# Performance work log

Measured on AMD Instinct MI355X. Metric: run time of the kernel, lower is better.

The kernel has to match this reference:

```python
import jax, jax.numpy as jnp
import numpy as np

D_MODEL = 1024
SCALE = float(np.sqrt(D_MODEL))


def setup_inputs() -> dict:
    key = jax.random.key(0)
    k1, k2, k3 = jax.random.split(key, 3)
    input_data = jax.random.normal(k1, (4, 2048, D_MODEL), dtype=jnp.float32)
    qk = jax.random.normal(k2, (D_MODEL, D_MODEL), dtype=jnp.float32) / SCALE
    ov = jax.random.normal(k3, (D_MODEL, D_MODEL), dtype=jnp.float32) / SCALE
    return {"input_data": input_data, "qk": qk, "ov": ov}


def reference(input_data, qk, ov):
    # input_data: [B, S, D]; qk, ov: [D, D]
    S = input_data.shape[1]
    # scores: [B, S, S] = (x @ qk) @ x^T / sqrt(D)
    scores = jnp.einsum("bsd,de,bte->bst", input_data, qk, input_data) / SCALE
    # causal mask: positions t > s get -inf (upper triangle, diagonal=1)
    causal = jnp.tril(jnp.ones((S, S), dtype=bool))
    scores = jnp.where(causal, scores, -jnp.inf)
    attn = jax.nn.softmax(scores, axis=-1)
    # A: [B, S, D] = attn @ x @ ov
    return jnp.einsum("bst,btd,de->bse", attn, input_data, ov)
```

## Files before the change

kernel.cpp:

```cpp
#include <hip/hip_runtime.h>
#include <hip/hip_bf16.h>
#include <cstdint>
#include <cstddef>
#include <type_traits>


using bf16 = __hip_bfloat16;
typedef __attribute__((ext_vector_type(8))) short short8;
typedef __attribute__((ext_vector_type(4))) float f32x4;

#define NB 4
#define SS 2048
#define DD 1024

__device__ __forceinline__ void async_lds16(const bf16* g, bf16* l) {
  __builtin_amdgcn_global_load_lds(
      (const __attribute__((address_space(1))) void*)g,
      (__attribute__((address_space(3))) void*)l,
      16, 0, 0);
}

struct alignas(8) bf16x4s { bf16 a, b, c, d; };

__global__ __launch_bounds__(256) void prep_kernel(const float* __restrict__ x,
                                                   bf16* __restrict__ xb,
                                                   const float* __restrict__ qk,
                                                   bf16* __restrict__ qkT,
                                                   const float* __restrict__ ov,
                                                   bf16* __restrict__ ovT,
                                                   float* __restrict__ l) {
  __shared__ bf16 tile[64][65];
  const int bx = blockIdx.x;
  if (bx < 8192) {
    int i = (bx * 256 + threadIdx.x) * 4;
    float4 v = *(const float4*)(x + i);
    bf16x4s o{__float2bfloat16(v.x), __float2bfloat16(v.y),
              __float2bfloat16(v.z), __float2bfloat16(v.w)};
    *(bf16x4s*)(xb + i) = o;
  } else if (bx < 8704) {
    const int idx = bx - 8192;
    const float* in = (idx & 256) ? ov : qk;
    bf16* out = (idx & 256) ? ovT : qkT;
    const int rem = idx & 255;
    const int tbx = (rem & 15) * 64;
    const int tby = (rem >> 4) * 64;
    const int tc = threadIdx.x & 63;
    const int tr = threadIdx.x >> 6;
#pragma unroll
    for (int r = tr; r < 64; r += 4)
      tile[tc][r] = __float2bfloat16(in[(size_t)(tby + r) * DD + tbx + tc]);
    __syncthreads();
#pragma unroll
    for (int r = tr; r < 64; r += 4)
      out[(size_t)(tbx + r) * DD + tby + tc] = tile[r][tc];
  } else {
    const int t = (bx - 8704) * 256 + threadIdx.x;
    f32x4 z = {0.f, 0.f, 0.f, 0.f};
    *(f32x4*)(l + t * 4) = z;
  }
}

template <int EPI>
__device__ __forceinline__ void gemm256_core(const bf16* __restrict__ Ab,
                                             const bf16* __restrict__ Bb,
                                             void* __restrict__ C,
                                             int N, int K, int m0, int n0, int nk,
                                             bf16* As, bf16* Bs,
                                             float* __restrict__ l) {
  const int lane = threadIdx.x & 63;
  const int wave = threadIdx.x >> 6;
  const int wr   = wave >> 2;
  const int wc   = wave & 3;
  const int quad = lane >> 4;
  const int r    = lane & 15;

  f32x4 acc[8][4];
#pragma unroll
  for (int i = 0; i < 8; ++i)
#pragma unroll
    for (int n = 0; n < 4; ++n) acc[i][n] = f32x4{0.f, 0.f, 0.f, 0.f};

  const int lrow = lane >> 3;
  const int lsw  = (lane & 7) ^ lrow;
  const long long a_lane = (long long)(m0 + wave * 8 + lrow) * K + lsw * 8;
  const long long b_lane = (long long)(n0 + wave * 8 + lrow) * K + lsw * 8;

  auto stageA = [&](int kt, int rnd, int buf) {
    async_lds16(Ab + a_lane + (long long)(rnd * 64) * K + (long long)kt * 64,
                As + buf * 16384 + (rnd * 64 + wave * 8) * 64);
  };
  auto stageB = [&](int kt, int rnd, int buf) {
    async_lds16(Bb + b_lane + (long long)(rnd * 64) * K + (long long)kt * 64,
                Bs + buf * 16384 + (rnd * 64 + wave * 8) * 64);
  };

  stageA(0, 0, 0); stageA(0, 2, 0);
  stageB(0, 0, 0); stageB(0, 1, 0); stageB(0, 2, 0); stageB(0, 3, 0);
  stageA(0, 1, 0); stageA(0, 3, 0);
  asm volatile("s_waitcnt vmcnt(2)" ::: "memory");
  asm volatile("s_barrier" ::: "memory");

  const int ca0 = (quad ^ (r & 7)) * 8;
  const int ca1 = ((4 + quad) ^ (r & 7)) * 8;

  for (int kt = 0; kt < nk; ++kt) {
    const int buf = kt & 1, nxt = buf ^ 1;
    const bool hn = (kt + 1 < nk);
    const bf16* Abuf = As + buf * 16384 + (wr * 128) * 64;
    const bf16* Bbuf = Bs + buf * 16384 + (wc * 64) * 64;

    auto phase = [&](auto RHC, int ca, auto&& stg, int wmode) {
      constexpr int RH = decltype(RHC)::value;
      short8 af[4], bfr[4];
#pragma unroll
      for (int m = 0; m < 4; ++m)
        af[m] = *(const short8*)(Abuf + (RH * 64 + m * 16 + r) * 64 + ca);
#pragma unroll
      for (int n = 0; n < 4; ++n)
        bfr[n] = *(const short8*)(Bbuf + (n * 16 + r) * 64 + ca);
      stg();
      asm volatile("s_barrier" ::: "memory");
      asm volatile("s_waitcnt lgkmcnt(0)" ::: "memory");
      __builtin_amdgcn_sched_barrier(0);
      __builtin_amdgcn_s_setprio(1);
#pragma unroll
      for (int m = 0; m < 4; ++m)
#pragma unroll
        for (int n = 0; n < 4; ++n)
          acc[RH * 4 + m][n] = __builtin_amdgcn_mfma_f32_16x16x32_bf16(
              af[m], bfr[n], acc[RH * 4 + m][n], 0, 0, 0);
      __builtin_amdgcn_s_setprio(0);
      if (wmode == 1) {
        if (hn) asm volatile("s_waitcnt vmcnt(2)" ::: "memory");
        else    asm volatile("s_waitcnt vmcnt(0)" ::: "memory");
      } else if (wmode == 2) {
        if (hn) asm volatile("s_waitcnt vmcnt(2)" ::: "memory");
      }
      asm volatile("s_barrier" ::: "memory");
    };

    phase(std::integral_constant<int, 0>{}, ca0,
          [&] { if (hn) { stageA(kt + 1, 0, nxt); stageA(kt + 1, 2, nxt); } }, 1);
    phase(std::integral_constant<int, 1>{}, ca0,
          [&] { if (hn) { stageB(kt + 1, 0, nxt); stageB(kt + 1, 1, nxt); } }, 0);
    phase(std::integral_constant<int, 0>{}, ca1,
          [&] { if (hn) { stageB(kt + 1, 2, nxt); stageB(kt + 1, 3, nxt); } }, 0);
    phase(std::integral_constant<int, 1>{}, ca1,
          [&] { if (hn) { stageA(kt + 1, 1, nxt); stageA(kt + 1, 3, nxt); } }, 2);
  }

#pragma unroll
  for (int i = 0; i < 8; ++i) {
    const int row0 = m0 + wr * 128 + i * 16 + quad * 4;
    if (EPI == 1) {
#pragma unroll
      for (int n = 0; n < 4; ++n) {
        const int col = n0 + wc * 64 + n * 16 + r;
#pragma unroll
        for (int q = 0; q < 4; ++q)
          ((bf16*)C)[(long long)(row0 + q) * N + col] = __float2bfloat16(acc[i][n][q]);
      }
    } else if (EPI == 2) {
      float qs[4] = {0.f, 0.f, 0.f, 0.f};
#pragma unroll
      for (int n = 0; n < 4; ++n) {
        const int col = n0 + wc * 64 + n * 16 + r;
#pragma unroll
        for (int q = 0; q < 4; ++q) {
          const int row = row0 + q;
          float v = (col <= row) ? __expf(acc[i][n][q] * 0.03125f) : 0.0f;
          ((bf16*)C)[(long long)row * N + col] = __float2bfloat16(v);
          qs[q] += v;
        }
      }
#pragma unroll
      for (int q = 0; q < 4; ++q) {
#pragma unroll
        for (int off = 1; off < 16; off <<= 1) qs[q] += __shfl_xor(qs[q], off, 64);
        if (r == 0) atomicAdd(&l[row0 + q], qs[q]);
      }
    } else {
      float rs[4];
#pragma unroll
      for (int q = 0; q < 4; ++q) rs[q] = 1.0f / l[row0 + q];
#pragma unroll
      for (int n = 0; n < 4; ++n) {
        const int col = n0 + wc * 64 + n * 16 + r;
#pragma unroll
        for (int q = 0; q < 4; ++q)
          ((float*)C)[(long long)(row0 + q) * N + col] = acc[i][n][q] * rs[q];
      }
    }
  }
}

__global__ __launch_bounds__(512, 2) void gemm_qv256(const bf16* __restrict__ xb,
                                                     const bf16* __restrict__ qkT,
                                                     const bf16* __restrict__ ovT,
                                                     bf16* __restrict__ Qb,
                                                     bf16* __restrict__ Vt) {
  extern __shared__ bf16 lds[];
  bf16* As = lds;
  bf16* Bs = lds + 32768;
  const long long SD = (long long)SS * DD;
  const int z = blockIdx.z;
  if (z < 4) {
    const int bn = blockIdx.x & 3, bm = blockIdx.x >> 2;
    gemm256_core<1>(xb + z * SD, qkT, Qb + z * SD, DD, DD, bm * 256, bn * 256, 16,
                    As, Bs, nullptr);
  } else {
    const int bm = blockIdx.x & 3, bn = blockIdx.x >> 2;
    gemm256_core<1>(ovT, xb + (z - 4) * SD, Vt + (z - 4) * SD, SS, DD, bm * 256, bn * 256, 16,
                    As, Bs, nullptr);
  }
}

__global__ __launch_bounds__(512, 2) void gemm_sc256(const bf16* __restrict__ Qb,
                                                     const bf16* __restrict__ xb,
                                                     bf16* __restrict__ P,
                                                     float* __restrict__ l) {
  extern __shared__ bf16 lds[];
  bf16* As = lds;
  bf16* Bs = lds + 32768;
  const long long SD = (long long)SS * DD;
  const long long SSQ = (long long)SS * SS;
  const int t = blockIdx.x;
  int bm = (int)((sqrtf(8.0f * (float)t + 1.0f) - 1.0f) * 0.5f);
  while ((bm + 1) * (bm + 2) / 2 <= t) ++bm;
  while (bm * (bm + 1) / 2 > t) --bm;
  const int bn = t - bm * (bm + 1) / 2;
  const int b = blockIdx.z;
  gemm256_core<2>(Qb + b * SD, xb + b * SD, P + b * SSQ, SS, DD, bm * 256, bn * 256, 16,
                  As, Bs, l + b * SS);
}

__global__ __launch_bounds__(512, 2) void gemm_pv256(const bf16* __restrict__ P,
                                                     const bf16* __restrict__ Vt,
                                                     const float* __restrict__ l,
                                                     float* __restrict__ out) {
  extern __shared__ bf16 lds[];
  bf16* As = lds;
  bf16* Bs = lds + 32768;
  const long long SD = (long long)SS * DD;
  const long long SSQ = (long long)SS * SS;
  const int bx = blockIdx.x & 3;
  const int bm = blockIdx.x >> 2;
  const int b = blockIdx.z;
  gemm256_core<3>(P + b * SSQ, Vt + b * SD, out + b * SD, DD, SS,
                  bm * 256, bx * 256, 4 * (bm + 1), As, Bs, (float*)l + b * SS);
}

extern "C" void kernel_launch(void* const* d_in, const int* in_sizes, int n_in,
                              void* d_out, int out_size, void* d_ws, size_t ws_size,
                              hipStream_t stream) {
  const float* x  = (const float*)d_in[0];
  const float* qk = (const float*)d_in[1];
  const float* ov = (const float*)d_in[2];
  float* out = (float*)d_out;

  char* ws = (char*)d_ws;
  const size_t MB = 1ull << 20;
  bf16*  xb  = (bf16*)(ws + 0);
  bf16*  qkT = (bf16*)(ws + 16 * MB);
  bf16*  ovT = (bf16*)(ws + 18 * MB);
  bf16*  Qb  = (bf16*)(ws + 20 * MB);
  bf16*  Vt  = (bf16*)(ws + 36 * MB);
  bf16*  P   = (bf16*)(ws + 52 * MB);
  float* l   = (float*)(ws + 84 * MB);

  static bool lds_opt_in = false;
  if (!lds_opt_in) {
    hipFuncSetAttribute((const void*)gemm_qv256,
                        hipFuncAttributeMaxDynamicSharedMemorySize, 131072);
    hipFuncSetAttribute((const void*)gemm_sc256,
                        hipFuncAttributeMaxDynamicSharedMemorySize, 131072);
    hipFuncSetAttribute((const void*)gemm_pv256,
                        hipFuncAttributeMaxDynamicSharedMemorySize, 131072);
    lds_opt_in = true;
  }

  prep_kernel<<<dim3(8712), 256, 0, stream>>>(x, xb, qk, qkT, ov, ovT, l);
  gemm_qv256<<<dim3(32, 1, 8), 512, 131072, stream>>>(xb, qkT, ovT, Qb, Vt);
  gemm_sc256<<<dim3(36, 1, 4), 512, 131072, stream>>>(Qb, xb, P, l);
  gemm_pv256<<<dim3(32, 1, 4), 512, 131072, stream>>>(P, Vt, l, out);
}
```

Before: 217.0 us.

## Triple-buffer A tiles in LDS to prefetch two k-steps ahead

Grows the A-operand LDS staging from two buffers to three, so A tiles are fetched two k-iterations ahead while B stays double-buffered. The per-phase staging schedule and vmcnt waits are reworked to match, and dynamic LDS grows to 160 KB per block. The aim is to hide more global-load latency behind MFMA work, at the cost of more LDS per block. That may cut occupancy: with launch_bounds(512,2) two blocks can no longer fit on a CU's LDS.

Result: slower. 221.8 us (+2.2%).

```diff
diff --git a/kernel.cpp b/kernel.cpp
--- a/kernel.cpp
+++ b/kernel.cpp
@@ -94,22 +94,30 @@
                 Bs + buf * 16384 + (rnd * 64 + wave * 8) * 64);
   };
 
-  stageA(0, 0, 0); stageA(0, 2, 0);
+  stageA(0, 0, 0); stageA(0, 2, 0); stageA(0, 1, 0); stageA(0, 3, 0);
   stageB(0, 0, 0); stageB(0, 1, 0); stageB(0, 2, 0); stageB(0, 3, 0);
-  stageA(0, 1, 0); stageA(0, 3, 0);
-  asm volatile("s_waitcnt vmcnt(2)" ::: "memory");
+  if (nk > 1) {
+    stageA(1, 0, 1); stageA(1, 2, 1); stageA(1, 1, 1); stageA(1, 3, 1);
+    asm volatile("s_waitcnt vmcnt(4)" ::: "memory");
+  } else {
+    asm volatile("s_waitcnt vmcnt(0)" ::: "memory");
+  }
   asm volatile("s_barrier" ::: "memory");
 
   const int ca0 = (quad ^ (r & 7)) * 8;
   const int ca1 = ((4 + quad) ^ (r & 7)) * 8;
 
+  int ba = 0;
   for (int kt = 0; kt < nk; ++kt) {
-    const int buf = kt & 1, nxt = buf ^ 1;
-    const bool hn = (kt + 1 < nk);
-    const bf16* Abuf = As + buf * 16384 + (wr * 128) * 64;
-    const bf16* Bbuf = Bs + buf * 16384 + (wc * 64) * 64;
-
-    auto phase = [&](auto RHC, int ca, auto&& stg, int wmode) {
+    const int bb  = kt & 1;
+    const int bb1 = bb ^ 1;
+    int ba2 = ba + 2; if (ba2 >= 3) ba2 -= 3;
+    const bool hnA = (kt + 2 < nk);
+    const bool hnB = (kt + 1 < nk);
+    const bf16* Abuf = As + ba * 16384 + (wr * 128) * 64;
+    const bf16* Bbuf = Bs + bb * 16384 + (wc * 64) * 64;
+
+    auto phase = [&](auto RHC, int ca, auto&& stg, bool tail) {
       constexpr int RH = decltype(RHC)::value;
       short8 af[4], bfr[4];
 #pragma unroll
@@ -130,23 +138,25 @@
           acc[RH * 4 + m][n] = __builtin_amdgcn_mfma_f32_16x16x32_bf16(
               af[m], bfr[n], acc[RH * 4 + m][n], 0, 0, 0);
       __builtin_amdgcn_s_setprio(0);
-      if (wmode == 1) {
-        if (hn) asm volatile("s_waitcnt vmcnt(2)" ::: "memory");
-        else    asm volatile("s_waitcnt vmcnt(0)" ::: "memory");
-      } else if (wmode == 2) {
-        if (hn) asm volatile("s_waitcnt vmcnt(2)" ::: "memory");
+      if (tail) {
+        if (hnA)      asm volatile("s_waitcnt vmcnt(2)" ::: "memory");
+        else if (hnB) asm volatile("s_waitcnt vmcnt(0)" ::: "memory");
       }
       asm volatile("s_barrier" ::: "memory");
     };
 
     phase(std::integral_constant<int, 0>{}, ca0,
-          [&] { if (hn) { stageA(kt + 1, 0, nxt); stageA(kt + 1, 2, nxt); } }, 1);
+          [&] {
+            if (hnA) { stageA(kt + 2, 0, ba2); stageA(kt + 2, 2, ba2); }
+            if (hnB) { stageB(kt + 1, 0, bb1); stageB(kt + 1, 1, bb1); }
+          }, false);
     phase(std::integral_constant<int, 1>{}, ca0,
-          [&] { if (hn) { stageB(kt + 1, 0, nxt); stageB(kt + 1, 1, nxt); } }, 0);
-    phase(std::integral_constant<int, 0>{}, ca1,
-          [&] { if (hn) { stageB(kt + 1, 2, nxt); stageB(kt + 1, 3, nxt); } }, 0);
+          [&] { if (hnB) { stageB(kt + 1, 2, bb1); stageB(kt + 1, 3, bb1); } }, false);
+    phase(std::integral_constant<int, 0>{}, ca1, [&] {}, false);
     phase(std::integral_constant<int, 1>{}, ca1,
-          [&] { if (hn) { stageA(kt + 1, 1, nxt); stageA(kt + 1, 3, nxt); } }, 2);
+          [&] { if (hnA) { stageA(kt + 2, 1, ba2); stageA(kt + 2, 3, ba2); } }, true);
+
+    if (++ba == 3) ba = 0;
   }
 
 #pragma unroll
@@ -201,7 +211,7 @@
                                                      bf16* __restrict__ Vt) {
   extern __shared__ bf16 lds[];
   bf16* As = lds;
-  bf16* Bs = lds + 32768;
+  bf16* Bs = lds + 49152;
   const long long SD = (long long)SS * DD;
   const int z = blockIdx.z;
   if (z < 4) {
@@ -221,7 +231,7 @@
                                                      float* __restrict__ l) {
   extern __shared__ bf16 lds[];
   bf16* As = lds;
-  bf16* Bs = lds + 32768;
+  bf16* Bs = lds + 49152;
   const long long SD = (long long)SS * DD;
   const long long SSQ = (long long)SS * SS;
   const int t = blockIdx.x;
@@ -240,7 +250,7 @@
                                                      float* __restrict__ out) {
   extern __shared__ bf16 lds[];
   bf16* As = lds;
-  bf16* Bs = lds + 32768;
+  bf16* Bs = lds + 49152;
   const long long SD = (long long)SS * DD;
   const long long SSQ = (long long)SS * SS;
   const int bx = blockIdx.x & 3;
@@ -271,16 +281,16 @@
   static bool lds_opt_in = false;
   if (!lds_opt_in) {
     hipFuncSetAttribute((const void*)gemm_qv256,
-                        hipFuncAttributeMaxDynamicSharedMemorySize, 131072);
+                        hipFuncAttributeMaxDynamicSharedMemorySize, 163840);
     hipFuncSetAttribute((const void*)gemm_sc256,
-                        hipFuncAttributeMaxDynamicSharedMemorySize, 131072);
+                        hipFuncAttributeMaxDynamicSharedMemorySize, 163840);
     hipFuncSetAttribute((const void*)gemm_pv256,
-                        hipFuncAttributeMaxDynamicSharedMemorySize, 131072);
+                        hipFuncAttributeMaxDynamicSharedMemorySize, 163840);
     lds_opt_in = true;
   }
 
   prep_kernel<<<dim3(8712), 256, 0, stream>>>(x, xb, qk, qkT, ov, ovT, l);
-  gemm_qv256<<<dim3(32, 1, 8), 512, 131072, stream>>>(xb, qkT, ovT, Qb, Vt);
-  gemm_sc256<<<dim3(36, 1, 4), 512, 131072, stream>>>(Qb, xb, P, l);
-  gemm_pv256<<<dim3(32, 1, 4), 512, 131072, stream>>>(P, Vt, l, out);
-}
+  gemm_qv256<<<dim3(32, 1, 8), 512, 163840, stream>>>(xb, qkT, ovT, Qb, Vt);
+  gemm_sc256<<<dim3(36, 1, 4), 512, 163840, stream>>>(Qb, xb, P, l);
+  gemm_pv256<<<dim3(32, 1, 4), 512, 163840, stream>>>(P, Vt, l, out);
+}
```

## Rewrite PV GEMM with 128-tile core and paired causal row blocks

Applied to the files above, without the earlier changes.

Replaces the 256x256 PV GEMM with a new 128x128 tile core using 256 threads, triple-buffered A and double-buffered B async LDS staging. Each block processes two complementary causal row tiles (row pr and 15-pr), so every block does the same total K work and the triangular imbalance disappears. The launch grows to 256 blocks, which gives more parallelism across CUs. In exchange, the smaller tiles reuse each loaded element less and the new pipeline code is more complex.

After: 192.7 us. 11.2% less time.

```diff
diff --git a/kernel.cpp b/kernel.cpp
--- a/kernel.cpp
+++ b/kernel.cpp
@@ -179,17 +179,108 @@
         for (int off = 1; off < 16; off <<= 1) qs[q] += __shfl_xor(qs[q], off, 64);
         if (r == 0) atomicAdd(&l[row0 + q], qs[q]);
       }
-    } else {
-      float rs[4];
-#pragma unroll
-      for (int q = 0; q < 4; ++q) rs[q] = 1.0f / l[row0 + q];
-#pragma unroll
-      for (int n = 0; n < 4; ++n) {
-        const int col = n0 + wc * 64 + n * 16 + r;
-#pragma unroll
-        for (int q = 0; q < 4; ++q)
-          ((float*)C)[(long long)(row0 + q) * N + col] = acc[i][n][q] * rs[q];
-      }
+    }
+  }
+}
+
+__device__ __forceinline__ void gemm128_core(const bf16* __restrict__ Ab,
+                                             const bf16* __restrict__ Bb,
+                                             float* __restrict__ C,
+                                             const float* __restrict__ l,
+                                             int N, int K, int m0, int n0, int nk,
+                                             bf16* As, bf16* Bs) {
+  const int lane = threadIdx.x & 63;
+  const int wave = threadIdx.x >> 6;
+  const int wr   = wave >> 1;
+  const int wc   = wave & 1;
+  const int quad = lane >> 4;
+  const int r    = lane & 15;
+
+  f32x4 acc[4][4];
+#pragma unroll
+  for (int m = 0; m < 4; ++m)
+#pragma unroll
+    for (int n = 0; n < 4; ++n) acc[m][n] = f32x4{0.f, 0.f, 0.f, 0.f};
+
+  const int lrow = lane >> 3;
+  const int lsw  = (lane & 7) ^ lrow;
+  const long long a_base = (long long)(m0 + wave * 32 + lrow) * K + lsw * 8;
+  const long long b_base = (long long)(n0 + wave * 32 + lrow) * K + lsw * 8;
+
+  auto stageA = [&](int kt, int buf) {
+#pragma unroll
+    for (int i = 0; i < 4; ++i)
+      async_lds16(Ab + a_base + (long long)(i * 8) * K + (long long)kt * 64,
+                  As + buf * 8192 + (wave * 32 + i * 8) * 64);
+  };
+  auto stageB = [&](int kt, int buf) {
+#pragma unroll
+    for (int i = 0; i < 4; ++i)
+      async_lds16(Bb + b_base + (long long)(i * 8) * K + (long long)kt * 64,
+                  Bs + buf * 8192 + (wave * 32 + i * 8) * 64);
+  };
+
+  stageB(0, 0); stageA(0, 0); stageA(1, 1);
+  asm volatile("s_waitcnt vmcnt(4)" ::: "memory");
+  asm volatile("s_barrier" ::: "memory");
+
+  const int ca0 = (quad ^ (r & 7)) * 8;
+  const int ca1 = ((4 + quad) ^ (r & 7)) * 8;
+
+  int ba = 0;
+  for (int kt = 0; kt < nk; ++kt) {
+    const int bb = kt & 1;
+    int ba2 = ba + 2; if (ba2 >= 3) ba2 -= 3;
+    const bool hA = (kt + 2 < nk), hB = (kt + 1 < nk);
+    const bf16* Abuf = As + ba * 8192;
+    const bf16* Bbuf = Bs + bb * 8192;
+
+    auto phase = [&](int ca, auto&& stg, bool tail) {
+      short8 af[4], bfr[4];
+#pragma unroll
+      for (int m = 0; m < 4; ++m)
+        af[m] = *(const short8*)(Abuf + (wr * 64 + m * 16 + r) * 64 + ca);
+#pragma unroll
+      for (int n = 0; n < 4; ++n)
+        bfr[n] = *(const short8*)(Bbuf + (wc * 64 + n * 16 + r) * 64 + ca);
+      stg();
+      asm volatile("s_barrier" ::: "memory");
+      asm volatile("s_waitcnt lgkmcnt(0)" ::: "memory");
+      __builtin_amdgcn_sched_barrier(0);
+      __builtin_amdgcn_s_setprio(1);
+#pragma unroll
+      for (int m = 0; m < 4; ++m)
+#pragma unroll
+        for (int n = 0; n < 4; ++n)
+          acc[m][n] = __builtin_amdgcn_mfma_f32_16x16x32_bf16(
+              af[m], bfr[n], acc[m][n], 0, 0, 0);
+      __builtin_amdgcn_s_setprio(0);
+      if (tail) {
+        if (hA)      asm volatile("s_waitcnt vmcnt(4)" ::: "memory");
+        else if (hB) asm volatile("s_waitcnt vmcnt(0)" ::: "memory");
+      }
+      asm volatile("s_barrier" ::: "memory");
+    };
+
+    phase(ca0, [&] { if (hB) stageB(kt + 1, bb ^ 1);
+                     if (hA) stageA(kt + 2, ba2); }, false);
+    phase(ca1, [&] {}, true);
+
+    if (++ba == 3) ba = 0;
+  }
+
+#pragma unroll
+  for (int m = 0; m < 4; ++m) {
+    const int row0 = m0 + wr * 64 + m * 16 + quad * 4;
+    float rs[4];
+#pragma unroll
+    for (int q = 0; q < 4; ++q) rs[q] = 1.0f / l[row0 + q];
+#pragma unroll
+    for (int n = 0; n < 4; ++n) {
+      const int col = n0 + wc * 64 + n * 16 + r;
+#pragma unroll
+      for (int q = 0; q < 4; ++q)
+        C[(long long)(row0 + q) * N + col] = acc[m][n][q] * rs[q];
     }
   }
 }
@@ -234,20 +325,25 @@
                   As, Bs, l + b * SS);
 }
 
-__global__ __launch_bounds__(512, 2) void gemm_pv256(const bf16* __restrict__ P,
+__global__ __launch_bounds__(256, 2) void gemm_pv128(const bf16* __restrict__ P,
                                                      const bf16* __restrict__ Vt,
                                                      const float* __restrict__ l,
                                                      float* __restrict__ out) {
   extern __shared__ bf16 lds[];
   bf16* As = lds;
-  bf16* Bs = lds + 32768;
+  bf16* Bs = lds + 24576;
   const long long SD = (long long)SS * DD;
   const long long SSQ = (long long)SS * SS;
-  const int bx = blockIdx.x & 3;
-  const int bm = blockIdx.x >> 2;
-  const int b = blockIdx.z;
-  gemm256_core<3>(P + b * SSQ, Vt + b * SD, out + b * SD, DD, SS,
-                  bm * 256, bx * 256, 4 * (bm + 1), As, Bs, (float*)l + b * SS);
+  const int c  = blockIdx.x & 7;
+  const int pr = blockIdx.x >> 3;
+  const int b  = blockIdx.z;
+  const int n0 = c * 128;
+  const int rL = 15 - pr;
+  gemm128_core(P + b * SSQ, Vt + b * SD, out + b * SD, (const float*)l + b * SS,
+               DD, SS, rL * 128, n0, 2 * (rL + 1), As, Bs);
+  __syncthreads();
+  gemm128_core(P + b * SSQ, Vt + b * SD, out + b * SD, (const float*)l + b * SS,
+               DD, SS, pr * 128, n0, 2 * (pr + 1), As, Bs);
 }
 
 extern "C" void kernel_launch(void* const* d_in, const int* in_sizes, int n_in,
@@ -274,13 +370,13 @@
                         hipFuncAttributeMaxDynamicSharedMemorySize, 131072);
     hipFuncSetAttribute((const void*)gemm_sc256,
                         hipFuncAttributeMaxDynamicSharedMemorySize, 131072);
-    hipFuncSetAttribute((const void*)gemm_pv256,
-                        hipFuncAttributeMaxDynamicSharedMemorySize, 131072);
+    hipFuncSetAttribute((const void*)gemm_pv128,
+                        hipFuncAttributeMaxDynamicSharedMemorySize, 81920);
     lds_opt_in = true;
   }
 
   prep_kernel<<<dim3(8712), 256, 0, stream>>>(x, xb, qk, qkT, ov, ovT, l);
   gemm_qv256<<<dim3(32, 1, 8), 512, 131072, stream>>>(xb, qkT, ovT, Qb, Vt);
   gemm_sc256<<<dim3(36, 1, 4), 512, 131072, stream>>>(Qb, xb, P, l);
-  gemm_pv256<<<dim3(32, 1, 4), 512, 131072, stream>>>(P, Vt, l, out);
-}
+  gemm_pv128<<<dim3(64, 1, 4), 256, 81920, stream>>>(P, Vt, l, out);
+}
```
